# Optimization experiments

Hardware: AMD Instinct MI355X
Metric: run time of the kernel (lower is better)

## Reference

```python
import jax, jax.numpy as jnp
import numpy as np

MIN_S = 0.05
MAX_S = 0.3
B, D = 16384, 2048
H = D // 4


def setup_inputs() -> dict:
    key = jax.random.key(0)
    k1, k2, k3 = jax.random.split(key, 3)
    x = jax.random.normal(k1, (B, D), dtype=jnp.float32)
    # sparsity predictor params (stored [in, out]); torch Linear default init scale
    s1 = 1.0 / np.sqrt(D)
    s2 = 1.0 / np.sqrt(H)
    W1 = jax.random.uniform(k2, (D, H), jnp.float32, -s1, s1)
    b1 = jnp.zeros((H,), jnp.float32)
    W2 = jax.random.uniform(k3, (H, 1), jnp.float32, -s2, s2)
    b2 = jnp.zeros((1,), jnp.float32)
    return {"x": x, "W1": W1, "b1": b1, "W2": W2, "b2": b2}


def reference(x, W1, b1, W2, b2):
    # sparsity predictor: Linear -> ReLU -> Linear -> Sigmoid, scaled to [min,max]
    h = jax.nn.relu(x @ W1 + b1)                         # [B, H]
    sig = jax.nn.sigmoid(h @ W2 + b2)                    # [B, 1]
    sparsity = MIN_S + (MAX_S - MIN_S) * sig             # [B, 1]

    d = x.shape[1]
    abs_x = jnp.abs(x)
    # per-row k = max(1, round(D * (1 - s))); torch uses Python round (half-even),
    # matching jnp.round semantics
    k = jnp.maximum(1, jnp.round(d * (1.0 - sparsity[:, 0])).astype(jnp.int32))  # [B]
    sorted_abs = jnp.sort(abs_x, axis=1)                 # [B, D] ascending
    threshold = jnp.take_along_axis(sorted_abs, (k - 1)[:, None], axis=1)        # [B, 1]

    mask = (abs_x > threshold).astype(x.dtype)           # [B, D]
    sparse_x = x * mask
    actual_sparsity = mask.sum(axis=1) / d               # [B]
    l1_reg = jnp.abs(sparse_x).sum(axis=1).mean()        # scalar
    return sparse_x, mask, sparsity, actual_sparsity, l1_reg
```

## Files before the change

### kernel.cpp

```cpp
#include <hip/hip_runtime.h>
#include <math.h>

#define B_ROWS 16384
#define D_DIM  2048
#define H_DIM  512

typedef __attribute__((ext_vector_type(8))) short  s16x8;
typedef __attribute__((ext_vector_type(4))) float  f32x4;

union U8 { unsigned short us[8]; s16x8 v; };

static __device__ __forceinline__ unsigned short f2bf(float f) {
    unsigned u = __float_as_uint(f);
    u += 0x7FFFu + ((u >> 16) & 1u);
    return (unsigned short)(u >> 16);
}

__global__ __launch_bounds__(256) void pack_w1(
    const float* __restrict__ W1, unsigned short* __restrict__ Wp)
{
    const int gid = blockIdx.x * 256 + threadIdx.x;
    const int ko = gid >> 9;
    const int n  = gid & 511;
    U8 h8, l8;
    #pragma unroll
    for (int j = 0; j < 8; ++j) {
        const float w = W1[(size_t)(ko * 8 + j) * H_DIM + n];
        const unsigned short h = f2bf(w);
        const float hf = __uint_as_float((unsigned)h << 16);
        h8.us[j] = h;
        l8.us[j] = f2bf(w - hf);
    }
    const int s    = ko >> 2;
    const int lane = (n & 15) | ((ko & 3) << 4);
    const int Nt   = n >> 4;
    const size_t baseH = ((((size_t)0 * 64 + s) * 32 + Nt) * 64 + lane) * 8;
    const size_t baseL = ((((size_t)1 * 64 + s) * 32 + Nt) * 64 + lane) * 8;
    *(s16x8*)(Wp + baseH) = h8.v;
    *(s16x8*)(Wp + baseL) = l8.v;
}

__global__ __launch_bounds__(256, 2) void predictor_gemm(
    const float* __restrict__ x, const unsigned short* __restrict__ Wp,
    const float* __restrict__ b1, const float* __restrict__ W2,
    double* __restrict__ logit)
{
    __shared__ __align__(16) unsigned short Abuf[2][2][4 * 64 * 8];

    const int tid = threadIdx.x;
    const int l   = tid & 63;
    const int Nw  = tid >> 6;
    const int bx  = blockIdx.x;
    const int by  = blockIdx.y;
    const int rowBase = bx * 64;

    const int sm = tid >> 2;
    const int sko = tid & 3;
    const float* xrow_p = x + (size_t)(rowBase + sm) * D_DIM + sko * 8;
    const int aMt   = sm >> 4;
    const int aLane = (sm & 15) | (sko << 4);
    unsigned short* aDstH[2] = {&Abuf[0][0][aMt * 512 + aLane * 8],
                                &Abuf[1][0][aMt * 512 + aLane * 8]};
    unsigned short* aDstL[2] = {&Abuf[0][1][aMt * 512 + aLane * 8],
                                &Abuf[1][1][aMt * 512 + aLane * 8]};

    const s16x8* WpV = (const s16x8*)Wp;
    const int NtBase = by * 16 + Nw * 4;

    f32x4 acc[4][4];
    #pragma unroll
    for (int mt = 0; mt < 4; ++mt)
        #pragma unroll
        for (int nt = 0; nt < 4; ++nt)
            acc[mt][nt] = {0.f, 0.f, 0.f, 0.f};

    float4 xa = *(const float4*)(xrow_p);
    float4 xb = *(const float4*)(xrow_p + 4);
    {
        U8 h8, l8;
        const float xv[8] = {xa.x, xa.y, xa.z, xa.w, xb.x, xb.y, xb.z, xb.w};
        #pragma unroll
        for (int i = 0; i < 8; ++i) {
            const unsigned short h = f2bf(xv[i]);
            h8.us[i] = h;
            l8.us[i] = f2bf(xv[i] - __uint_as_float((unsigned)h << 16));
        }
        *(s16x8*)aDstH[0] = h8.v;
        *(s16x8*)aDstL[0] = l8.v;
    }
    s16x8 Bh[4], Bl[4];
    #pragma unroll
    for (int nt = 0; nt < 4; ++nt) {
        Bh[nt] = WpV[((0 * 64 + 0) * 32 + NtBase + nt) * 64 + l];
        Bl[nt] = WpV[((1 * 64 + 0) * 32 + NtBase + nt) * 64 + l];
    }
    __syncthreads();

    for (int s = 0; s < 64; ++s) {
        const int cur = s & 1, nxt = cur ^ 1;
        s16x8 BhN[4], BlN[4];
        if (s < 63) {
            #pragma unroll
            for (int nt = 0; nt < 4; ++nt) {
                BhN[nt] = WpV[((0 * 64 + (s + 1)) * 32 + NtBase + nt) * 64 + l];
                BlN[nt] = WpV[((1 * 64 + (s + 1)) * 32 + NtBase + nt) * 64 + l];
            }
            xa = *(const float4*)(xrow_p + (s + 1) * 32);
            xb = *(const float4*)(xrow_p + (s + 1) * 32 + 4);
        }

        s16x8 Ah[4], Al[4];
        #pragma unroll
        for (int mt = 0; mt < 4; ++mt) {
            Ah[mt] = *(const s16x8*)&Abuf[cur][0][mt * 512 + l * 8];
            Al[mt] = *(const s16x8*)&Abuf[cur][1][mt * 512 + l * 8];
        }

        #pragma unroll
        for (int mt = 0; mt < 4; ++mt)
            #pragma unroll
            for (int nt = 0; nt < 4; ++nt) {
                acc[mt][nt] = __builtin_amdgcn_mfma_f32_16x16x32_bf16(Ah[mt], Bh[nt], acc[mt][nt], 0, 0, 0);
                acc[mt][nt] = __builtin_amdgcn_mfma_f32_16x16x32_bf16(Al[mt], Bh[nt], acc[mt][nt], 0, 0, 0);
                acc[mt][nt] = __builtin_amdgcn_mfma_f32_16x16x32_bf16(Ah[mt], Bl[nt], acc[mt][nt], 0, 0, 0);
                acc[mt][nt] = __builtin_amdgcn_mfma_f32_16x16x32_bf16(Al[mt], Bl[nt], acc[mt][nt], 0, 0, 0);
            }

        if (s < 63) {
            U8 h8, l8;
            const float xv[8] = {xa.x, xa.y, xa.z, xa.w, xb.x, xb.y, xb.z, xb.w};
            #pragma unroll
            for (int i = 0; i < 8; ++i) {
                const unsigned short h = f2bf(xv[i]);
                h8.us[i] = h;
                l8.us[i] = f2bf(xv[i] - __uint_as_float((unsigned)h << 16));
            }
            *(s16x8*)aDstH[nxt] = h8.v;
            *(s16x8*)aDstL[nxt] = l8.v;
            #pragma unroll
            for (int nt = 0; nt < 4; ++nt) { Bh[nt] = BhN[nt]; Bl[nt] = BlN[nt]; }
        }
        __syncthreads();
    }

    float  b1v[4];
    double w2v[4];
    #pragma unroll
    for (int nt = 0; nt < 4; ++nt) {
        const int j = by * 256 + (Nw * 4 + nt) * 16 + (l & 15);
        b1v[nt] = b1[j];
        w2v[nt] = (double)W2[j];
    }
    #pragma unroll
    for (int mt = 0; mt < 4; ++mt)
        #pragma unroll
        for (int reg = 0; reg < 4; ++reg) {
            double p = 0.0;
            #pragma unroll
            for (int nt = 0; nt < 4; ++nt) {
                const float h = acc[mt][nt][reg] + b1v[nt];
                if (h > 0.0f) p = fma((double)h, w2v[nt], p);
            }
            #pragma unroll
            for (int m2 = 1; m2 < 16; m2 <<= 1) p += __shfl_xor(p, m2, 64);
            if ((l & 15) == 0)
                atomicAdd(&logit[rowBase + mt * 16 + ((l >> 4) & 3) * 4 + reg], p);
        }
}

__global__ __launch_bounds__(256) void select_and_write(
    const float* __restrict__ x, const float* __restrict__ b2,
    const double* __restrict__ logit,
    float* __restrict__ out_sparse, float* __restrict__ out_mask,
    float* __restrict__ out_sparsity, float* __restrict__ out_actual,
    double* __restrict__ l1rows)
{
    __shared__ int hist[4][1024];

    const int tid = threadIdx.x;
    const int w = tid >> 6, l = tid & 63;
    const int row = blockIdx.x * 4 + w;
    int* hw = hist[w];

    const float4* x4 = (const float4*)(x + (size_t)row * D_DIM);
    float4 vv[8];
    #pragma unroll
    for (int i = 0; i < 8; ++i) vv[i] = x4[i * 64 + l];

    const double L = logit[row] + (double)b2[0];
    const double sig = 1.0 / (1.0 + exp(-L));
    const double s = 0.05 + 0.25 * sig;
    int k = (int)rint(2048.0 * (1.0 - s));
    if (k < 1) k = 1;
    if (k > 2048) k = 2048;
    if (l == 0) out_sparsity[row] = (float)s;

    int krem = k;
    unsigned prefix = 0;

    #pragma unroll
    for (int pass = 0; pass < 4; ++pass) {
        const int shift = 24 - pass * 8;
        const unsigned pmask = (pass == 0) ? 0u : (0xFFFFFFFFu << (shift + 8));

        #pragma unroll
        for (int j = 0; j < 4; ++j)
            ((int4*)hw)[l + 64 * j] = int4{0, 0, 0, 0};
        __builtin_amdgcn_wave_barrier();
        __threadfence_block();

        #pragma unroll
        for (int i = 0; i < 8; ++i) {
            const float qq[4] = {vv[i].x, vv[i].y, vv[i].z, vv[i].w};
            #pragma unroll
            for (int c = 0; c < 4; ++c) {
                const unsigned ub = __float_as_uint(qq[c]) & 0x7FFFFFFFu;
                if (pass == 0 || (ub & pmask) == prefix)
                    atomicAdd(&hw[((ub >> shift) & 255) * 4 + (l & 3)], 1);
            }
        }
        __builtin_amdgcn_wave_barrier();
        __threadfence_block();

        int b_[4], tot = 0;
        #pragma unroll
        for (int j = 0; j < 4; ++j) {
            const int4 c4 = ((const int4*)hw)[4 * l + j];
            b_[j] = c4.x + c4.y + c4.z + c4.w;
            tot += b_[j];
        }
        int sc = tot;
        #pragma unroll
        for (int off = 1; off < 64; off <<= 1) {
            const int n = __shfl_up(sc, off);
            if (l >= off) sc += n;
        }
        int cum = sc - tot;
        int found = 0;
        #pragma unroll
        for (int j = 0; j < 4; ++j) {
            if (krem > cum && krem <= cum + b_[j])
                found = ((4 * l + j) << 12) | (krem - cum);
            cum += b_[j];
        }
        #pragma unroll
        for (int m2 = 1; m2 < 64; m2 <<= 1) found |= __shfl_xor(found, m2);
        prefix |= ((unsigned)(found >> 12)) << shift;
        krem = found & 0xFFF;
    }
    const unsigned thr = prefix;

    float4* os4 = (float4*)(out_sparse + (size_t)row * D_DIM);
    float4* om4 = (float4*)(out_mask   + (size_t)row * D_DIM);
    int cnt = 0;
    double lp = 0.0;
    #pragma unroll
    for (int i = 0; i < 8; ++i) {
        const float qq[4] = {vv[i].x, vv[i].y, vv[i].z, vv[i].w};
        float sq[4], mq[4];
        #pragma unroll
        for (int c = 0; c < 4; ++c) {
            const unsigned ub = __float_as_uint(qq[c]) & 0x7FFFFFFFu;
            const bool keep = (ub > thr);
            mq[c] = keep ? 1.0f : 0.0f;
            sq[c] = keep ? qq[c] : 0.0f;
            cnt += keep ? 1 : 0;
            if (keep) lp += (double)fabsf(qq[c]);
        }
        os4[i * 64 + l] = float4{sq[0], sq[1], sq[2], sq[3]};
        om4[i * 64 + l] = float4{mq[0], mq[1], mq[2], mq[3]};
    }
    #pragma unroll
    for (int m2 = 1; m2 < 64; m2 <<= 1) {
        lp  += __shfl_xor(lp, m2);
        cnt += __shfl_xor(cnt, m2);
    }
    if (l == 0) {
        l1rows[row] = lp;
        out_actual[row] = (float)cnt * (1.0f / 2048.0f);
    }
}

__global__ __launch_bounds__(256) void finalize_l1(
    const double* __restrict__ l1rows, float* __restrict__ out_l1)
{
    __shared__ double sh[256];
    double s = 0.0;
    for (int i = threadIdx.x; i < B_ROWS; i += 256) s += l1rows[i];
    sh[threadIdx.x] = s;
    __syncthreads();
    for (int st = 128; st > 0; st >>= 1) {
        if (threadIdx.x < st) sh[threadIdx.x] += sh[threadIdx.x + st];
        __syncthreads();
    }
    if (threadIdx.x == 0) out_l1[0] = (float)(sh[0] / (double)B_ROWS);
}

extern "C" void kernel_launch(void* const* d_in, const int* in_sizes, int n_in,
                              void* d_out, int out_size, void* d_ws, size_t ws_size,
                              hipStream_t stream) {
    const float* x  = (const float*)d_in[0];
    const float* W1 = (const float*)d_in[1];
    const float* b1 = (const float*)d_in[2];
    const float* W2 = (const float*)d_in[3];
    const float* b2 = (const float*)d_in[4];

    float* out = (float*)d_out;
    float* out_sparse   = out;
    float* out_mask     = out + (size_t)B_ROWS * D_DIM;
    float* out_sparsity = out + 2ull * B_ROWS * D_DIM;
    float* out_actual   = out_sparsity + B_ROWS;
    float* out_l1       = out_actual + B_ROWS;

    double* logit  = (double*)d_ws;
    double* l1rows = logit + B_ROWS;
    unsigned short* Wp = (unsigned short*)(l1rows + B_ROWS);

    hipMemsetAsync(d_ws, 0, (size_t)B_ROWS * sizeof(double), stream);

    pack_w1<<<512, 256, 0, stream>>>(W1, Wp);
    dim3 g1(B_ROWS / 64, 2);
    predictor_gemm<<<g1, 256, 0, stream>>>(x, Wp, b1, W2, logit);
    select_and_write<<<B_ROWS / 4, 256, 0, stream>>>(x, b2, logit, out_sparse, out_mask,
                                                     out_sparsity, out_actual, l1rows);
    finalize_l1<<<1, 256, 0, stream>>>(l1rows, out_l1);
}
```

Before: 496.6 us.

## Pre-pack x into split-bf16 MFMA layout and drop LDS staging in predictor GEMM

A new pack_x kernel converts x once into bf16 hi/lo fragments laid out in MFMA lane order. The GEMM then loads A fragments straight from global memory with register double-buffering, so the LDS buffer and per-step barriers go away. Each 512-thread block now covers all 512 hidden columns, which removes the duplicate read of x across the old blockIdx.y split. The lo*lo MFMA term is also dropped, cutting matrix work by a quarter at a small accuracy cost. The price is an extra pass that writes and re-reads about 128 MB of packed x, placed in workspace or, if that is too small, in the mask output buffer.

```diff
diff --git a/kernel.cpp b/kernel.cpp
--- a/kernel.cpp
+++ b/kernel.cpp
@@ -40,32 +40,48 @@
     *(s16x8*)(Wp + baseL) = l8.v;
 }
 
-__global__ __launch_bounds__(256, 2) void predictor_gemm(
-    const float* __restrict__ x, const unsigned short* __restrict__ Wp,
+__global__ __launch_bounds__(256) void pack_x(
+    const float* __restrict__ x, unsigned short* __restrict__ Xp)
+{
+    const int gid = blockIdx.x * 256 + threadIdx.x;
+    const int l  = gid & 63;
+    const int s  = (gid >> 6) & 63;
+    const int rt = gid >> 12;
+    const float* p = x + (size_t)(rt * 16 + (l & 15)) * D_DIM + s * 32 + (l >> 4) * 8;
+    const float4 a = *(const float4*)p;
+    const float4 b = *(const float4*)(p + 4);
+    U8 h8, l8;
+    const float xv[8] = {a.x, a.y, a.z, a.w, b.x, b.y, b.z, b.w};
+    #pragma unroll
+    for (int j = 0; j < 8; ++j) {
+        const unsigned short h = f2bf(xv[j]);
+        h8.us[j] = h;
+        l8.us[j] = f2bf(xv[j] - __uint_as_float((unsigned)h << 16));
+    }
+    const size_t base = (size_t)gid * 8;
+    *(s16x8*)(Xp + base) = h8.v;
+    *(s16x8*)(Xp + 33554432ull + base) = l8.v;
+}
+
+__global__ __launch_bounds__(512, 2) void predictor_gemm(
+    const unsigned short* __restrict__ Xp, const unsigned short* __restrict__ Wp,
     const float* __restrict__ b1, const float* __restrict__ W2,
     double* __restrict__ logit)
 {
-    __shared__ __align__(16) unsigned short Abuf[2][2][4 * 64 * 8];
-
     const int tid = threadIdx.x;
     const int l   = tid & 63;
     const int Nw  = tid >> 6;
     const int bx  = blockIdx.x;
-    const int by  = blockIdx.y;
     const int rowBase = bx * 64;
-
-    const int sm = tid >> 2;
-    const int sko = tid & 3;
-    const float* xrow_p = x + (size_t)(rowBase + sm) * D_DIM + sko * 8;
-    const int aMt   = sm >> 4;
-    const int aLane = (sm & 15) | (sko << 4);
-    unsigned short* aDstH[2] = {&Abuf[0][0][aMt * 512 + aLane * 8],
-                                &Abuf[1][0][aMt * 512 + aLane * 8]};
-    unsigned short* aDstL[2] = {&Abuf[0][1][aMt * 512 + aLane * 8],
-                                &Abuf[1][1][aMt * 512 + aLane * 8]};
-
+    const int NtBase  = Nw * 4;
+
+    const s16x8* XpV = (const s16x8*)Xp;
     const s16x8* WpV = (const s16x8*)Wp;
-    const int NtBase = by * 16 + Nw * 4;
+
+    const s16x8* aH = XpV + ((size_t)(bx * 4) * 64) * 64 + l;
+    const s16x8* aL = aH + 1024ull * 64 * 64;
+    const s16x8* bH = WpV + (size_t)NtBase * 64 + l;
+    const s16x8* bL = bH + 64ull * 32 * 64;
 
     f32x4 acc[4][4];
     #pragma unroll
@@ -74,46 +90,31 @@
         for (int nt = 0; nt < 4; ++nt)
             acc[mt][nt] = {0.f, 0.f, 0.f, 0.f};
 
-    float4 xa = *(const float4*)(xrow_p);
-    float4 xb = *(const float4*)(xrow_p + 4);
-    {
-        U8 h8, l8;
-        const float xv[8] = {xa.x, xa.y, xa.z, xa.w, xb.x, xb.y, xb.z, xb.w};
-        #pragma unroll
-        for (int i = 0; i < 8; ++i) {
-            const unsigned short h = f2bf(xv[i]);
-            h8.us[i] = h;
-            l8.us[i] = f2bf(xv[i] - __uint_as_float((unsigned)h << 16));
-        }
-        *(s16x8*)aDstH[0] = h8.v;
-        *(s16x8*)aDstL[0] = l8.v;
-    }
-    s16x8 Bh[4], Bl[4];
+    s16x8 Ah[4], Al[4], Bh[4], Bl[4];
+    #pragma unroll
+    for (int mt = 0; mt < 4; ++mt) {
+        Ah[mt] = aH[(size_t)mt * 4096];
+        Al[mt] = aL[(size_t)mt * 4096];
+    }
     #pragma unroll
     for (int nt = 0; nt < 4; ++nt) {
-        Bh[nt] = WpV[((0 * 64 + 0) * 32 + NtBase + nt) * 64 + l];
-        Bl[nt] = WpV[((1 * 64 + 0) * 32 + NtBase + nt) * 64 + l];
-    }
-    __syncthreads();
+        Bh[nt] = bH[nt * 64];
+        Bl[nt] = bL[nt * 64];
+    }
 
     for (int s = 0; s < 64; ++s) {
-        const int cur = s & 1, nxt = cur ^ 1;
-        s16x8 BhN[4], BlN[4];
+        s16x8 AhN[4], AlN[4], BhN[4], BlN[4];
         if (s < 63) {
             #pragma unroll
+            for (int mt = 0; mt < 4; ++mt) {
+                AhN[mt] = aH[(size_t)mt * 4096 + (s + 1) * 64];
+                AlN[mt] = aL[(size_t)mt * 4096 + (s + 1) * 64];
+            }
+            #pragma unroll
             for (int nt = 0; nt < 4; ++nt) {
-                BhN[nt] = WpV[((0 * 64 + (s + 1)) * 32 + NtBase + nt) * 64 + l];
-                BlN[nt] = WpV[((1 * 64 + (s + 1)) * 32 + NtBase + nt) * 64 + l];
-            }
-            xa = *(const float4*)(xrow_p + (s + 1) * 32);
-            xb = *(const float4*)(xrow_p + (s + 1) * 32 + 4);
-        }
-
-        s16x8 Ah[4], Al[4];
-        #pragma unroll
-        for (int mt = 0; mt < 4; ++mt) {
-            Ah[mt] = *(const s16x8*)&Abuf[cur][0][mt * 512 + l * 8];
-            Al[mt] = *(const s16x8*)&Abuf[cur][1][mt * 512 + l * 8];
+                BhN[nt] = bH[(s + 1) * 2048 + nt * 64];
+                BlN[nt] = bL[(s + 1) * 2048 + nt * 64];
+            }
         }
 
         #pragma unroll
@@ -123,31 +124,22 @@
                 acc[mt][nt] = __builtin_amdgcn_mfma_f32_16x16x32_bf16(Ah[mt], Bh[nt], acc[mt][nt], 0, 0, 0);
                 acc[mt][nt] = __builtin_amdgcn_mfma_f32_16x16x32_bf16(Al[mt], Bh[nt], acc[mt][nt], 0, 0, 0);
                 acc[mt][nt] = __builtin_amdgcn_mfma_f32_16x16x32_bf16(Ah[mt], Bl[nt], acc[mt][nt], 0, 0, 0);
-                acc[mt][nt] = __builtin_amdgcn_mfma_f32_16x16x32_bf16(Al[mt], Bl[nt], acc[mt][nt], 0, 0, 0);
             }
 
         if (s < 63) {
-            U8 h8, l8;
-            const float xv[8] = {xa.x, xa.y, xa.z, xa.w, xb.x, xb.y, xb.z, xb.w};
-            #pragma unroll
-            for (int i = 0; i < 8; ++i) {
-                const unsigned short h = f2bf(xv[i]);
-                h8.us[i] = h;
-                l8.us[i] = f2bf(xv[i] - __uint_as_float((unsigned)h << 16));
-            }
-            *(s16x8*)aDstH[nxt] = h8.v;
-            *(s16x8*)aDstL[nxt] = l8.v;
-            #pragma unroll
-            for (int nt = 0; nt < 4; ++nt) { Bh[nt] = BhN[nt]; Bl[nt] = BlN[nt]; }
-        }
-        __syncthreads();
+            #pragma unroll
+            for (int i = 0; i < 4; ++i) {
+                Ah[i] = AhN[i]; Al[i] = AlN[i];
+                Bh[i] = BhN[i]; Bl[i] = BlN[i];
+            }
+        }
     }
 
     float  b1v[4];
     double w2v[4];
     #pragma unroll
     for (int nt = 0; nt < 4; ++nt) {
-        const int j = by * 256 + (Nw * 4 + nt) * 16 + (l & 15);
+        const int j = (NtBase + nt) * 16 + (l & 15);
         b1v[nt] = b1[j];
         w2v[nt] = (double)W2[j];
     }
@@ -316,11 +308,20 @@
     double* l1rows = logit + B_ROWS;
     unsigned short* Wp = (unsigned short*)(l1rows + B_ROWS);
 
+    const size_t fixedBytes = 2ull * B_ROWS * sizeof(double)
+                            + 2ull * 64 * 32 * 512 * sizeof(unsigned short);
+    const size_t XP_BYTES = 2ull * B_ROWS * D_DIM * sizeof(unsigned short);
+    unsigned short* Xp;
+    if (ws_size >= fixedBytes + XP_BYTES)
+        Xp = (unsigned short*)((char*)d_ws + fixedBytes);
+    else
+        Xp = (unsigned short*)out_mask;
+
     hipMemsetAsync(d_ws, 0, (size_t)B_ROWS * sizeof(double), stream);
 
     pack_w1<<<512, 256, 0, stream>>>(W1, Wp);
-    dim3 g1(B_ROWS / 64, 2);
-    predictor_gemm<<<g1, 256, 0, stream>>>(x, Wp, b1, W2, logit);
+    pack_x<<<16384, 256, 0, stream>>>(x, Xp);
+    predictor_gemm<<<256, 512, 0, stream>>>(Xp, Wp, b1, W2, logit);
     select_and_write<<<B_ROWS / 4, 256, 0, stream>>>(x, b2, logit, out_sparse, out_mask,
                                                      out_sparsity, out_actual, l1rows);
     finalize_l1<<<1, 256, 0, stream>>>(l1rows, out_l1);
```

Result: slower. 567.5 us (+14.3%).

## Cover all hidden columns per block with 8 waves and drop lo*lo MFMA

Applied to the files above, without the earlier changes.

The predictor GEMM block grows from 4 to 8 waves so a single block covers all 512 hidden units, replacing the 2-wide grid over column halves. Each x row tile is now loaded and split into bf16 hi/lo once instead of twice, and each thread stages 4 floats instead of 8. The lo*lo product term of the split-bf16 emulation is removed, cutting MFMA work by a quarter. This slightly lowers accuracy of the logit, and the larger blocks may change occupancy.

```diff
diff --git a/kernel.cpp b/kernel.cpp
--- a/kernel.cpp
+++ b/kernel.cpp
@@ -9,6 +9,7 @@
 typedef __attribute__((ext_vector_type(4))) float  f32x4;
 
 union U8 { unsigned short us[8]; s16x8 v; };
+union U4 { unsigned short us[4]; short4 v; };
 
 static __device__ __forceinline__ unsigned short f2bf(float f) {
     unsigned u = __float_as_uint(f);
@@ -40,32 +41,28 @@
     *(s16x8*)(Wp + baseL) = l8.v;
 }
 
-__global__ __launch_bounds__(256, 2) void predictor_gemm(
+__global__ __launch_bounds__(512, 2) void predictor_gemm(
     const float* __restrict__ x, const unsigned short* __restrict__ Wp,
     const float* __restrict__ b1, const float* __restrict__ W2,
     double* __restrict__ logit)
 {
-    __shared__ __align__(16) unsigned short Abuf[2][2][4 * 64 * 8];
+    __shared__ __align__(16) unsigned short Abuf[2][2][2048];
 
     const int tid = threadIdx.x;
     const int l   = tid & 63;
     const int Nw  = tid >> 6;
     const int bx  = blockIdx.x;
-    const int by  = blockIdx.y;
     const int rowBase = bx * 64;
-
-    const int sm = tid >> 2;
-    const int sko = tid & 3;
-    const float* xrow_p = x + (size_t)(rowBase + sm) * D_DIM + sko * 8;
-    const int aMt   = sm >> 4;
-    const int aLane = (sm & 15) | (sko << 4);
-    unsigned short* aDstH[2] = {&Abuf[0][0][aMt * 512 + aLane * 8],
-                                &Abuf[1][0][aMt * 512 + aLane * 8]};
-    unsigned short* aDstL[2] = {&Abuf[0][1][aMt * 512 + aLane * 8],
-                                &Abuf[1][1][aMt * 512 + aLane * 8]};
+    const int NtBase  = Nw * 4;
+
+    const int sm = tid >> 3;
+    const int sh = tid & 7;
+    const float* xp = x + (size_t)(rowBase + sm) * D_DIM + sh * 4;
+    const int stIdx = (sm >> 4) * 512 + (((sm & 15) | ((sh >> 1) << 4)) << 3) + (sh & 1) * 4;
+    unsigned short* stH[2] = {&Abuf[0][0][stIdx], &Abuf[1][0][stIdx]};
+    unsigned short* stL[2] = {&Abuf[0][1][stIdx], &Abuf[1][1][stIdx]};
 
     const s16x8* WpV = (const s16x8*)Wp;
-    const int NtBase = by * 16 + Nw * 4;
 
     f32x4 acc[4][4];
     #pragma unroll
@@ -74,19 +71,18 @@
         for (int nt = 0; nt < 4; ++nt)
             acc[mt][nt] = {0.f, 0.f, 0.f, 0.f};
 
-    float4 xa = *(const float4*)(xrow_p);
-    float4 xb = *(const float4*)(xrow_p + 4);
     {
-        U8 h8, l8;
-        const float xv[8] = {xa.x, xa.y, xa.z, xa.w, xb.x, xb.y, xb.z, xb.w};
-        #pragma unroll
-        for (int i = 0; i < 8; ++i) {
-            const unsigned short h = f2bf(xv[i]);
-            h8.us[i] = h;
-            l8.us[i] = f2bf(xv[i] - __uint_as_float((unsigned)h << 16));
-        }
-        *(s16x8*)aDstH[0] = h8.v;
-        *(s16x8*)aDstL[0] = l8.v;
+        const float4 v = *(const float4*)(xp);
+        const float xv[4] = {v.x, v.y, v.z, v.w};
+        U4 h4, l4;
+        #pragma unroll
+        for (int j = 0; j < 4; ++j) {
+            const unsigned short h = f2bf(xv[j]);
+            h4.us[j] = h;
+            l4.us[j] = f2bf(xv[j] - __uint_as_float((unsigned)h << 16));
+        }
+        *(short4*)stH[0] = h4.v;
+        *(short4*)stL[0] = l4.v;
     }
     s16x8 Bh[4], Bl[4];
     #pragma unroll
@@ -99,14 +95,14 @@
     for (int s = 0; s < 64; ++s) {
         const int cur = s & 1, nxt = cur ^ 1;
         s16x8 BhN[4], BlN[4];
+        float4 xn;
         if (s < 63) {
             #pragma unroll
             for (int nt = 0; nt < 4; ++nt) {
                 BhN[nt] = WpV[((0 * 64 + (s + 1)) * 32 + NtBase + nt) * 64 + l];
                 BlN[nt] = WpV[((1 * 64 + (s + 1)) * 32 + NtBase + nt) * 64 + l];
             }
-            xa = *(const float4*)(xrow_p + (s + 1) * 32);
-            xb = *(const float4*)(xrow_p + (s + 1) * 32 + 4);
+            xn = *(const float4*)(xp + (s + 1) * 32);
         }
 
         s16x8 Ah[4], Al[4];
@@ -123,20 +119,19 @@
                 acc[mt][nt] = __builtin_amdgcn_mfma_f32_16x16x32_bf16(Ah[mt], Bh[nt], acc[mt][nt], 0, 0, 0);
                 acc[mt][nt] = __builtin_amdgcn_mfma_f32_16x16x32_bf16(Al[mt], Bh[nt], acc[mt][nt], 0, 0, 0);
                 acc[mt][nt] = __builtin_amdgcn_mfma_f32_16x16x32_bf16(Ah[mt], Bl[nt], acc[mt][nt], 0, 0, 0);
-                acc[mt][nt] = __builtin_amdgcn_mfma_f32_16x16x32_bf16(Al[mt], Bl[nt], acc[mt][nt], 0, 0, 0);
             }
 
         if (s < 63) {
-            U8 h8, l8;
-            const float xv[8] = {xa.x, xa.y, xa.z, xa.w, xb.x, xb.y, xb.z, xb.w};
-            #pragma unroll
-            for (int i = 0; i < 8; ++i) {
-                const unsigned short h = f2bf(xv[i]);
-                h8.us[i] = h;
-                l8.us[i] = f2bf(xv[i] - __uint_as_float((unsigned)h << 16));
-            }
-            *(s16x8*)aDstH[nxt] = h8.v;
-            *(s16x8*)aDstL[nxt] = l8.v;
+            const float xv[4] = {xn.x, xn.y, xn.z, xn.w};
+            U4 h4, l4;
+            #pragma unroll
+            for (int j = 0; j < 4; ++j) {
+                const unsigned short h = f2bf(xv[j]);
+                h4.us[j] = h;
+                l4.us[j] = f2bf(xv[j] - __uint_as_float((unsigned)h << 16));
+            }
+            *(short4*)stH[nxt] = h4.v;
+            *(short4*)stL[nxt] = l4.v;
             #pragma unroll
             for (int nt = 0; nt < 4; ++nt) { Bh[nt] = BhN[nt]; Bl[nt] = BlN[nt]; }
         }
@@ -147,7 +142,7 @@
     double w2v[4];
     #pragma unroll
     for (int nt = 0; nt < 4; ++nt) {
-        const int j = by * 256 + (Nw * 4 + nt) * 16 + (l & 15);
+        const int j = (NtBase + nt) * 16 + (l & 15);
         b1v[nt] = b1[j];
         w2v[nt] = (double)W2[j];
     }
@@ -319,8 +314,7 @@
     hipMemsetAsync(d_ws, 0, (size_t)B_ROWS * sizeof(double), stream);
 
     pack_w1<<<512, 256, 0, stream>>>(W1, Wp);
-    dim3 g1(B_ROWS / 64, 2);
-    predictor_gemm<<<g1, 256, 0, stream>>>(x, Wp, b1, W2, logit);
+    predictor_gemm<<<B_ROWS / 64, 512, 0, stream>>>(x, Wp, b1, W2, logit);
     select_and_write<<<B_ROWS / 4, 256, 0, stream>>>(x, b2, logit, out_sparse, out_mask,
                                                      out_sparsity, out_actual, l1rows);
     finalize_l1<<<1, 256, 0, stream>>>(l1rows, out_l1);
```

After: 505.7 us. No clear change (+1.8%).
